# Performance work log

Hardware: AMD Instinct MI355X
Metric: run time of the kernel (lower is better)

Reference implementation:

```python
import jax, jax.numpy as jnp
import numpy as np

B, N, D, L = 4, 16384, 1024, 4
NEG = -10000.0


def setup_inputs() -> dict:
    key = jax.random.key(0)
    k1, k2, k3, k4, k5 = jax.random.split(key, 5)
    xs = jax.random.normal(k1, (B, N, D), dtype=jnp.float32)
    valid = jax.random.randint(k2, (B, N), 0, 2).astype(jnp.bool_)
    # ensure at least one valid instance per bag
    valid = valid.at[:, 0].set(True)
    w1 = jax.random.normal(k3, (D, 1), dtype=jnp.float32) * (1.0 / np.sqrt(D))
    w2 = jax.random.normal(k4, (D, 1), dtype=jnp.float32) * (1.0 / np.sqrt(D))
    wf = jax.random.normal(k5, (L, D), dtype=jnp.float32) * (1.0 / np.sqrt(D))
    return {"xs": xs, "valid": valid, "w1": w1, "w2": w2, "wf": wf}


def reference(xs, valid, w1, w2, wf):
    # gated attention scores: tanh(x w1) * sigmoid(x w2)  -> [B, N]
    a = jnp.tanh(xs @ w1)[..., 0] * jax.nn.sigmoid(xs @ w2)[..., 0]
    # padding mask fill (matches a[~valid] = -10000)
    a = jnp.where(valid, a, NEG)
    att = jax.nn.softmax(a, axis=-1)            # [B, N]
    z = jnp.einsum('bn,bnd->bd', att, xs)       # weighted-sum pooling
    return z @ wf.T                              # [B, L]
```

## Files before the change

### kernel.cpp

```cpp
#include <hip/hip_runtime.h>
#include <hip/hip_bf16.h>
#include <math.h>


#define NB   4
#define NN   16384
#define DD   1024
#define LL   4
#define NBLK 256
#define RPB  (NN / NBLK)
#define RPW  (RPB / 4)

struct POut { float pd[LL]; float s; float pad[3]; };

__device__ __forceinline__ float wave_reduce(float v) {
    #pragma unroll
    for (int off = 32; off > 0; off >>= 1) v += __shfl_xor(v, off, 64);
    return v;
}

__device__ __forceinline__ float fast_rcp(float x) {
    return __builtin_amdgcn_rcpf(x);
}

__device__ __forceinline__ int popnext(unsigned& m) {
    if (m == 0u) return -1;
    const int i = (int)__builtin_ctz(m);
    m &= m - 1u;
    return i;
}

__global__ __launch_bounds__(256, 4) void abmil_main(
    const float* __restrict__ xs, const void* __restrict__ valid,
    const float* __restrict__ w1, const float* __restrict__ w2,
    const float* __restrict__ wf, POut* __restrict__ parts) {
    const int blk  = blockIdx.x;
    const int bag  = blockIdx.y;
    const int tid  = threadIdx.x;
    const int wave = tid >> 6;
    const int lane = tid & 63;

    __shared__ int   nflag[2];
    __shared__ float comb[4][LL];
    __shared__ float scomb[4];

    if (tid == 0) { nflag[0] = 0; nflag[1] = 0; }
    __syncthreads();
    {
        const uint4 xq = ((const uint4*)valid)[tid];
        const unsigned w[4] = {xq.x, xq.y, xq.z, xq.w};
        int bi = 0, bf = 0;
        #pragma unroll
        for (int j = 0; j < 4; ++j) {
            if (w[j] != 0u && w[j] != 1u) bi = 1;
            if (w[j] != 0u && w[j] != 0x3F800000u) bf = 1;
        }
        if (bi) atomicOr(&nflag[0], 1);
        if (bf) atomicOr(&nflag[1], 1);
    }
    __syncthreads();
    const int mode = (!nflag[0]) ? 1 : ((!nflag[1]) ? 2 : 0);

    const float4* w1v = (const float4*)w1;
    const float4* w2v = (const float4*)w2;
    float4 w1r[4], w2r[4];
    #pragma unroll
    for (int k = 0; k < 4; ++k) {
        w1r[k] = w1v[k * 64 + lane];
        w2r[k] = w2v[k * 64 + lane];
    }

    const int n0 = blk * RPB + wave * RPW;
    int flag = 0;
    if (lane < RPW) {
        const size_t idx = (size_t)bag * NN + n0 + lane;
        if (mode == 1)      flag = ((const int*)valid)[idx] != 0;
        else if (mode == 2) flag = ((const float*)valid)[idx] != 0.0f;
        else                flag = ((const unsigned char*)valid)[idx] != 0;
    }
    unsigned m = (unsigned)(__ballot(flag) & 0xFFFFull);

    float s = 0.0f;
    float4 z[4];
    #pragma unroll
    for (int k = 0; k < 4; ++k) z[k] = make_float4(0.f, 0.f, 0.f, 0.f);

    const float4* xbase = (const float4*)(xs + (size_t)bag * NN * DD);

    auto loadrow = [&](float4 (&xr)[4], int idx) {
        if (idx >= 0) {
            const float4* xp = xbase + (size_t)(n0 + idx) * (DD / 4);
            #pragma unroll
            for (int k = 0; k < 4; ++k) xr[k] = xp[k * 64 + lane];
        }
    };
    auto comprow = [&](const float4 (&xr)[4]) {
        float d1 = 0.f, d2 = 0.f;
        #pragma unroll
        for (int k = 0; k < 4; ++k) {
            d1 += xr[k].x * w1r[k].x + xr[k].y * w1r[k].y +
                  xr[k].z * w1r[k].z + xr[k].w * w1r[k].w;
            d2 += xr[k].x * w2r[k].x + xr[k].y * w2r[k].y +
                  xr[k].z * w2r[k].z + xr[k].w * w2r[k].w;
        }
        #pragma unroll
        for (int off = 32; off > 0; off >>= 1) {
            d1 += __shfl_xor(d1, off, 64);
            d2 += __shfl_xor(d2, off, 64);
        }
        const float e  = __expf(-2.0f * fabsf(d1));
        const float t  = copysignf((1.0f - e) * fast_rcp(1.0f + e), d1);
        const float sg = fast_rcp(1.0f + __expf(-d2));
        const float p  = __expf(t * sg);
        s += p;
        #pragma unroll
        for (int k = 0; k < 4; ++k) {
            z[k].x += p * xr[k].x; z[k].y += p * xr[k].y;
            z[k].z += p * xr[k].z; z[k].w += p * xr[k].w;
        }
    };

    float4 xA[4], xB[4];
    int iA = popnext(m), iB = popnext(m);
    loadrow(xA, iA); loadrow(xB, iB);
    for (;;) {
        if (iA < 0) break;
        comprow(xA); iA = popnext(m); loadrow(xA, iA);
        if (iB < 0) break;
        comprow(xB); iB = popnext(m); loadrow(xB, iB);
    }

    const float4* wfv = (const float4*)wf;
    float pl[LL] = {0.f, 0.f, 0.f, 0.f};
    #pragma unroll
    for (int l = 0; l < LL; ++l) {
        #pragma unroll
        for (int k = 0; k < 4; ++k) {
            const float4 wv = wfv[l * 256 + k * 64 + lane];
            pl[l] += z[k].x * wv.x + z[k].y * wv.y +
                     z[k].z * wv.z + z[k].w * wv.w;
        }
    }
    #pragma unroll
    for (int l = 0; l < LL; ++l) pl[l] = wave_reduce(pl[l]);
    if (lane == 0) {
        #pragma unroll
        for (int l = 0; l < LL; ++l) comb[wave][l] = pl[l];
        scomb[wave] = s;
    }
    __syncthreads();

    POut* po = &parts[(size_t)bag * NBLK + blk];
    if (tid < LL)
        po->pd[tid] = comb[0][tid] + comb[1][tid] + comb[2][tid] + comb[3][tid];
    if (tid == LL)
        po->s = scomb[0] + scomb[1] + scomb[2] + scomb[3];
}

__global__ __launch_bounds__(256) void abmil_finish(
    const POut* __restrict__ parts, float* __restrict__ out) {
    const int bag  = threadIdx.x >> 6;
    const int lane = threadIdx.x & 63;

    float pd[LL] = {0.f, 0.f, 0.f, 0.f};
    float s = 0.0f;
    #pragma unroll
    for (int j = 0; j < NBLK / 64; ++j) {
        const POut* p = &parts[(size_t)bag * NBLK + j * 64 + lane];
        #pragma unroll
        for (int l = 0; l < LL; ++l) pd[l] += p->pd[l];
        s += p->s;
    }
    #pragma unroll
    for (int l = 0; l < LL; ++l) pd[l] = wave_reduce(pd[l]);
    s = wave_reduce(s);
    if (lane == 0) {
        #pragma unroll
        for (int l = 0; l < LL; ++l) out[bag * LL + l] = pd[l] / s;
    }
}

extern "C" void kernel_launch(void* const* d_in, const int* in_sizes, int n_in,
                              void* d_out, int out_size, void* d_ws, size_t ws_size,
                              hipStream_t stream) {
    const float* xs    = (const float*)d_in[0];
    const void*  valid = d_in[1];
    const float* w1    = (const float*)d_in[2];
    const float* w2    = (const float*)d_in[3];
    const float* wf    = (const float*)d_in[4];
    float* out = (float*)d_out;

    POut* parts = (POut*)d_ws;

    dim3 g0(NBLK, NB);
    abmil_main<<<g0, 256, 0, stream>>>(xs, valid, w1, w2, wf, parts);
    abmil_finish<<<1, 256, 0, stream>>>(parts, out);
}
```

Measured before the change: 34.53 us.

## Fuse finish kernel via atomic accumulation and last-block reduction; shrink rows per block

Replaces the second reduction kernel with global atomicAdd accumulation plus a done-counter so the last block computes the final outputs. It also halves rows per block, doubling the grid to 2048 blocks, and shrinks the valid-dtype detection to a single wave ballot over 16 words. The aim is to remove a kernel launch and improve load balance, at the cost of a memset launch, float atomic contention and order-dependent float sums. The shorter dtype probe is less robust.

```diff
diff --git a/kernel.cpp b/kernel.cpp
--- a/kernel.cpp
+++ b/kernel.cpp
@@ -7,11 +7,10 @@
 #define NN   16384
 #define DD   1024
 #define LL   4
-#define NBLK 256
-#define RPB  (NN / NBLK)
-#define RPW  (RPB / 4)
-
-struct POut { float pd[LL]; float s; float pad[3]; };
+#define RPB  32
+#define RPW  8
+#define GX   (NN / RPB)
+#define NBLK (GX * NB)
 
 __device__ __forceinline__ float wave_reduce(float v) {
     #pragma unroll
@@ -30,36 +29,23 @@
     return i;
 }
 
+struct Accum { float pd[NB * LL]; float s[NB]; unsigned done; };
+
 __global__ __launch_bounds__(256, 4) void abmil_main(
     const float* __restrict__ xs, const void* __restrict__ valid,
     const float* __restrict__ w1, const float* __restrict__ w2,
-    const float* __restrict__ wf, POut* __restrict__ parts) {
+    const float* __restrict__ wf, Accum* __restrict__ acc,
+    float* __restrict__ out) {
     const int blk  = blockIdx.x;
     const int bag  = blockIdx.y;
     const int tid  = threadIdx.x;
     const int wave = tid >> 6;
     const int lane = tid & 63;
 
-    __shared__ int   nflag[2];
-    __shared__ float comb[4][LL];
-    __shared__ float scomb[4];
-
-    if (tid == 0) { nflag[0] = 0; nflag[1] = 0; }
-    __syncthreads();
-    {
-        const uint4 xq = ((const uint4*)valid)[tid];
-        const unsigned w[4] = {xq.x, xq.y, xq.z, xq.w};
-        int bi = 0, bf = 0;
-        #pragma unroll
-        for (int j = 0; j < 4; ++j) {
-            if (w[j] != 0u && w[j] != 1u) bi = 1;
-            if (w[j] != 0u && w[j] != 0x3F800000u) bf = 1;
-        }
-        if (bi) atomicOr(&nflag[0], 1);
-        if (bf) atomicOr(&nflag[1], 1);
-    }
-    __syncthreads();
-    const int mode = (!nflag[0]) ? 1 : ((!nflag[1]) ? 2 : 0);
+    const unsigned wd = ((const unsigned*)valid)[lane & 15];
+    const unsigned long long bi = __ballot(wd != 0u && wd != 1u);
+    const unsigned long long bf = __ballot(wd != 0u && wd != 0x3F800000u);
+    const int mode = (bi == 0ull) ? 1 : ((bf == 0ull) ? 2 : 0);
 
     const float4* w1v = (const float4*)w1;
     const float4* w2v = (const float4*)w2;
@@ -78,7 +64,7 @@
         else if (mode == 2) flag = ((const float*)valid)[idx] != 0.0f;
         else                flag = ((const unsigned char*)valid)[idx] != 0;
     }
-    unsigned m = (unsigned)(__ballot(flag) & 0xFFFFull);
+    unsigned m = (unsigned)(__ballot(flag) & 0xFFull);
 
     float s = 0.0f;
     float4 z[4];
@@ -143,6 +129,10 @@
     }
     #pragma unroll
     for (int l = 0; l < LL; ++l) pl[l] = wave_reduce(pl[l]);
+
+    __shared__ float comb[4][LL];
+    __shared__ float scomb[4];
+    __shared__ int   lastf;
     if (lane == 0) {
         #pragma unroll
         for (int l = 0; l < LL; ++l) comb[wave][l] = pl[l];
@@ -150,33 +140,25 @@
     }
     __syncthreads();
 
-    POut* po = &parts[(size_t)bag * NBLK + blk];
     if (tid < LL)
-        po->pd[tid] = comb[0][tid] + comb[1][tid] + comb[2][tid] + comb[3][tid];
+        atomicAdd(&acc->pd[bag * LL + tid],
+                  comb[0][tid] + comb[1][tid] + comb[2][tid] + comb[3][tid]);
     if (tid == LL)
-        po->s = scomb[0] + scomb[1] + scomb[2] + scomb[3];
-}
+        atomicAdd(&acc->s[bag], scomb[0] + scomb[1] + scomb[2] + scomb[3]);
+    if (tid <= LL) __threadfence();
+    __syncthreads();
 
-__global__ __launch_bounds__(256) void abmil_finish(
-    const POut* __restrict__ parts, float* __restrict__ out) {
-    const int bag  = threadIdx.x >> 6;
-    const int lane = threadIdx.x & 63;
+    if (tid == 0) {
+        const unsigned r = atomicAdd(&acc->done, 1u);
+        lastf = (r == (unsigned)(NBLK - 1));
+    }
+    __syncthreads();
 
-    float pd[LL] = {0.f, 0.f, 0.f, 0.f};
-    float s = 0.0f;
-    #pragma unroll
-    for (int j = 0; j < NBLK / 64; ++j) {
-        const POut* p = &parts[(size_t)bag * NBLK + j * 64 + lane];
-        #pragma unroll
-        for (int l = 0; l < LL; ++l) pd[l] += p->pd[l];
-        s += p->s;
-    }
-    #pragma unroll
-    for (int l = 0; l < LL; ++l) pd[l] = wave_reduce(pd[l]);
-    s = wave_reduce(s);
-    if (lane == 0) {
-        #pragma unroll
-        for (int l = 0; l < LL; ++l) out[bag * LL + l] = pd[l] / s;
+    if (lastf && tid < NB * LL) {
+        __threadfence();
+        const float pd = atomicAdd(&acc->pd[tid], 0.0f);
+        const float sv = atomicAdd(&acc->s[tid >> 2], 0.0f);
+        out[tid] = pd / sv;
     }
 }
 
@@ -189,10 +171,10 @@
     const float* w2    = (const float*)d_in[3];
     const float* wf    = (const float*)d_in[4];
     float* out = (float*)d_out;
+    Accum* acc = (Accum*)d_ws;
 
-    POut* parts = (POut*)d_ws;
+    hipMemsetAsync(d_ws, 0, sizeof(Accum), stream);
 
-    dim3 g0(NBLK, NB);
-    abmil_main<<<g0, 256, 0, stream>>>(xs, valid, w1, w2, wf, parts);
-    abmil_finish<<<1, 256, 0, stream>>>(parts, out);
+    dim3 g0(GX, NB);
+    abmil_main<<<g0, 256, 0, stream>>>(xs, valid, w1, w2, wf, acc, out);
 }
```

After: 100.1 us. 2.9x slower.
